# Kernel optimization log

Hardware: AMD Instinct MI355X
Metric: run time of the kernel (lower is better)

## Reference

```python
import jax, jax.numpy as jnp
import numpy as np

B, CIN, COUT, K, IH, IW = 2, 32, 32, 9, 256, 256
OH, OW = 512, 512


def setup_inputs() -> dict:
    key = jax.random.key(0)
    k0, k1, k2, k3 = jax.random.split(key, 4)
    stdv = 1.0 / np.sqrt(CIN * K)
    x = jax.random.normal(k0, (B, CIN, IH, IW), jnp.float32)
    weight = jax.random.uniform(k1, (CIN, COUT, K), jnp.float32, -stdv, stdv)
    bias = jax.random.uniform(k2, (COUT,), jnp.float32, -stdv, stdv)
    # continuous (x, y) coords into the OUTPUT plane; keep strictly inside so x0+1/y0+1 are valid
    sm = jax.random.uniform(k3, (IH, IW, K, 2), jnp.float32)
    scale = jnp.array([(OW - 1) * 0.999, (OH - 1) * 0.999], jnp.float32)
    sample_map = sm * scale
    return {"x": x, "weight": weight, "bias": bias, "sample_map": sample_map, "oh": OH, "ow": OW}


def reference(x, weight, bias, sample_map, oh, ow):
    Bb, Cin, Ih, Iw = x.shape
    Cout = weight.shape[1]
    Kk = weight.shape[2]
    P = Ih * Iw
    xf = x.reshape(Bb, Cin, P)
    # per-kernel-tap weight transform of every input pixel: [B, Cout, K, P]
    contrib = jnp.einsum('bip,iok->bokp', xf, weight)

    sx = sample_map[..., 0].reshape(P, Kk).T  # [K, P] x-coords in output
    sy = sample_map[..., 1].reshape(P, Kk).T  # [K, P] y-coords in output
    x0f = jnp.floor(sx)
    y0f = jnp.floor(sy)
    dx = sx - x0f
    dy = sy - y0f
    x0 = jnp.clip(x0f.astype(jnp.int32), 0, ow - 1)
    y0 = jnp.clip(y0f.astype(jnp.int32), 0, oh - 1)
    x1 = jnp.clip(x0 + 1, 0, ow - 1)
    y1 = jnp.clip(y0 + 1, 0, oh - 1)

    # bilinear splat weights and flat output indices for the 4 corners: [4, K, P]
    w = jnp.stack([(1 - dx) * (1 - dy), dx * (1 - dy), (1 - dx) * dy, dx * dy], 0)
    idx = jnp.stack([y0 * ow + x0, y0 * ow + x1, y1 * ow + x0, y1 * ow + x1], 0)

    vals = contrib[:, :, None, :, :] * w[None, None, :, :, :]  # [B, Cout, 4, K, P]
    out = jnp.zeros((Bb, Cout, oh * ow), vals.dtype).at[:, :, idx].add(vals)
    return out.reshape(Bb, Cout, oh, ow) + bias[None, :, None, None]
```

## Files before the change

kernel.cpp:

```cpp
#include <hip/hip_runtime.h>
#include <hip/hip_fp16.h>

#define CIN 32
#define COUT 32
#define KK 9
#define PIX 65536
#define OH 512
#define OW 512
#define OHOW (OH*OW)
#define NCH 64
#define TW 16
#define TH 4
#define TPX (TW*TH)
#define NTX (OW/TW)
#define NTY (OH/TH)
#define NTILE (NTX*NTY)
#define NBIN NTILE
#define NPK (PIX*KK)
#define CAP 384

#define OFF_CNT 0
#define OFF_WT  (256*1024)
#define OFF_ENT (512*1024)
#define OFF_CB  (OFF_ENT + (size_t)NBIN*CAP*8)
#define WS_NEED (OFF_CB + (size_t)NPK*NCH*2)

typedef __bf16    bf16x8 __attribute__((ext_vector_type(8)));
typedef _Float16  f16x8  __attribute__((ext_vector_type(8)));
typedef float     f32x4  __attribute__((ext_vector_type(4)));

__device__ __forceinline__ unsigned short f2h(float v)
{
    return __half_as_ushort(__float2half_rn(v));
}

__device__ __forceinline__ void corners(float sx, float sy,
    int& x0, int& y0, int& x1, int& y1, float& dx, float& dy)
{
    const float x0f = floorf(sx), y0f = floorf(sy);
    dx = sx - x0f; dy = sy - y0f;
    x0 = min(max((int)x0f, 0), OW - 1);
    y0 = min(max((int)y0f, 0), OH - 1);
    x1 = min(x0 + 1, OW - 1);
    y1 = min(y0 + 1, OH - 1);
}

__global__ __launch_bounds__(256) void k_wtb(
    const float* __restrict__ w, __bf16* __restrict__ wth, __bf16* __restrict__ wtl)
{
    const int t = blockIdx.x * 256 + threadIdx.x;
    if (t < KK * COUT * CIN) {
        const int i = t & 31;
        const int o = (t >> 5) & 31;
        const int k = t >> 10;
        const float v = w[(i * COUT + o) * KK + k];
        const __bf16 h = (__bf16)v;
        wth[t] = h;
        wtl[t] = (__bf16)(v - (float)h);
    }
}

__global__ __launch_bounds__(256, 1) void k_contrib4(
    const float* __restrict__ x, const __bf16* __restrict__ wth,
    const __bf16* __restrict__ wtl, const float* __restrict__ smap,
    unsigned short* __restrict__ cb, unsigned* __restrict__ cnt,
    uint2* __restrict__ ent)
{
    __shared__ __align__(16) unsigned short patch[4][2][16][72];
    const int tid = threadIdx.x, lane = tid & 63;
    const int wu = __builtin_amdgcn_readfirstlane(tid >> 6);
    const int p0 = blockIdx.x * 64;
    const int colp = lane & 15;
    const int q    = lane >> 4;
    const int cig  = q * 8;

    unsigned aS[3][4], aA[3][4], aR[3][4], aW[3];
    #pragma unroll
    for (int it = 0; it < 3; ++it) {
        const int idx = tid + it * 256;
        const bool vit = idx < 576;
        const int t = min(p0 * KK + idx, NPK - 1);
        const float sx = smap[2 * t], sy = smap[2 * t + 1];
        int x0, y0, x1, y1; float dx, dy;
        corners(sx, sy, x0, y0, x1, y1, dx, dy);
        const int g0 = x0 >> 4, g1 = x1 >> 4;
        const int t0 = y0 >> 2, t1 = y1 >> 2;
        aW[it] = (unsigned)f2h(dx) | ((unsigned)f2h(dy) << 16);
        const bool dg = (g1 != g0), dt = (t1 != t0);
        const bool cond[4] = { vit, vit && dg, vit && dt, vit && dg && dt };
        const int  tys[4]  = { t0, t0, t1, t1 };
        const int  gss[4]  = { g0, g1, g0, g1 };
        #pragma unroll
        for (int e = 0; e < 4; ++e) {
            unsigned slot = 0xFFFFFFFFu;
            const int bin = tys[e] * 32 + gss[e];
            const unsigned lxb = (unsigned)(x0 - gss[e] * TW + 1);
            const unsigned lyb = (unsigned)(y0 - tys[e] * TH + 1);
            if (cond[e]) slot = atomicAdd(&cnt[bin * 16], 1u);
            aS[it][e] = slot;
            aA[it][e] = (unsigned)bin * CAP;
            aR[it][e] = (unsigned)t | (lxb << 20) | (lyb << 25);
        }
    }

    bf16x8 xh[2], xl[2];
    #pragma unroll
    for (int b = 0; b < 2; ++b) {
        const int p = p0 + wu * 16 + colp;
        #pragma unroll
        for (int j = 0; j < 8; ++j) {
            const float v = x[(size_t)(b * 32 + cig + j) * PIX + p];
            const __bf16 h = (__bf16)v;
            xh[b][j] = h;
            xl[b][j] = (__bf16)(v - (float)h);
        }
    }

    const int pxr = lane >> 2, cc = lane & 3;
    for (int k = 0; k < KK; ++k) {
        const int kb = k & 1;
        const __bf16* wb = wth + k * (COUT * CIN);
        const __bf16* lb = wtl + k * (COUT * CIN);
        bf16x8 wh[2], wl[2];
        #pragma unroll
        for (int oh = 0; oh < 2; ++oh) {
            wh[oh] = *(const bf16x8*)(wb + (oh * 16 + colp) * 32 + cig);
            wl[oh] = *(const bf16x8*)(lb + (oh * 16 + colp) * 32 + cig);
        }
        #pragma unroll
        for (int cg = 0; cg < 4; ++cg) {
            const int b = cg >> 1, oh = cg & 1;
            f32x4 a = {0.f, 0.f, 0.f, 0.f};
            a = __builtin_amdgcn_mfma_f32_16x16x32_bf16(wh[oh], xh[b], a, 0, 0, 0);
            a = __builtin_amdgcn_mfma_f32_16x16x32_bf16(wl[oh], xh[b], a, 0, 0, 0);
            a = __builtin_amdgcn_mfma_f32_16x16x32_bf16(wh[oh], xl[b], a, 0, 0, 0);
            const unsigned d0 = (unsigned)f2h(a[0]) | ((unsigned)f2h(a[1]) << 16);
            const unsigned d1 = (unsigned)f2h(a[2]) | ((unsigned)f2h(a[3]) << 16);
            *(uint2*)&patch[wu][kb][colp][cg * 16 + q * 4] = make_uint2(d0, d1);
        }
        const uint4 a0 = *(const uint4*)&patch[wu][kb][pxr][cc * 8];
        const uint4 a1 = *(const uint4*)&patch[wu][kb][pxr][32 + cc * 8];
        unsigned short* dst = cb + (size_t)(p0 + wu * 16 + pxr) * 576 + k * 64 + cc * 8;
        *(uint4*)dst        = a0;
        *(uint4*)(dst + 32) = a1;
    }

    #pragma unroll
    for (int it = 0; it < 3; ++it) {
        #pragma unroll
        for (int e = 0; e < 4; ++e) {
            if (aS[it][e] < CAP)
                ent[(size_t)aA[it][e] + aS[it][e]] = make_uint2(aR[it][e], aW[it]);
        }
    }
}

__global__ __launch_bounds__(256, 4) void k_gather(
    const unsigned short* __restrict__ cb, const uint2* __restrict__ ent,
    const unsigned* __restrict__ cnt, const float* __restrict__ bias,
    float* __restrict__ out)
{
    __shared__ __align__(16) unsigned char smem[32768];
    const int tid = threadIdx.x, lane = tid & 63;
    const int wv = __builtin_amdgcn_readfirstlane(tid >> 6);
    const int bt = blockIdx.x;
    const int tx0 = (bt & 31) * TW;
    const int ty0 = (bt >> 5) * TH;

    const unsigned count = min(cnt[bt * 16], (unsigned)CAP);
    const uint2* eb = ent + (size_t)bt * CAP;
    const int nb = (int)(count + 63) >> 6;

    f32x4 acc[4] = {{0.f,0.f,0.f,0.f},{0.f,0.f,0.f,0.f},
                    {0.f,0.f,0.f,0.f},{0.f,0.f,0.f,0.f}};

    for (int it = 0; it <= nb; ++it) {
        const int bb = it & 1;
        unsigned short* Wb = (unsigned short*)(smem + bb * 8192);
        unsigned short* Cv = (unsigned short*)(smem + 16384 + bb * 8192);
        if (it < nb) {
            uint4* wq = (uint4*)Wb;
            const uint4 z = make_uint4(0u, 0u, 0u, 0u);
            wq[tid] = z; wq[tid + 256] = z;
        }
        __syncthreads();

        unsigned short u[16];
        if (it < nb) {
            {
                const int eL = tid >> 2, cn = tid & 3;
                const unsigned idx = (unsigned)(it * 64 + eL);
                if (idx < count) {
                    const uint2 r = eb[idx];
                    const int lx = (int)((r.x >> 20) & 31) - 1 + (cn & 1);
                    const int ly = (int)((r.x >> 25) & 7) - 1 + (cn >> 1);
                    if (((unsigned)lx < TW) & ((unsigned)ly < TH)) {
                        const float dx = __half2float(__ushort_as_half((unsigned short)(r.y & 0xFFFF)));
                        const float dy = __half2float(__ushort_as_half((unsigned short)(r.y >> 16)));
                        const float wx = (cn & 1) ? dx : 1.f - dx;
                        const float wy = (cn >> 1) ? dy : 1.f - dy;
                        const int px = ly * TW + lx;
                        Wb[px * 64 + (eL ^ ((px & 7) << 3))] = f2h(wx * wy);
                    }
                }
            }
            #pragma unroll
            for (int j = 0; j < 16; ++j) {
                const unsigned idx = (unsigned)(it * 64 + wv * 16 + j);
                unsigned short v = 0;
                if (idx < count) {
                    const unsigned row = eb[idx].x & 0xFFFFFu;
                    v = cb[((size_t)row << 6) + lane];
                }
                u[j] = v;
            }
        }
        if (it > 0) {
            const int pb = bb ^ 1;
            const unsigned short* Wp = (const unsigned short*)(smem + pb * 8192);
            const unsigned short* Cp = (const unsigned short*)(smem + 16384 + pb * 8192);
            const int m = lane & 15, kh = lane >> 4;
            const int px = wv * 16 + m;
            f16x8 af[2];
            #pragma unroll
            for (int kc = 0; kc < 2; ++kc)
                af[kc] = *(const f16x8*)(Wp + px * 64 + (((kc * 4 + kh) ^ (px & 7)) << 3));
            #pragma unroll
            for (int n = 0; n < 4; ++n) {
                const int ch = n * 16 + m;
                #pragma unroll
                for (int kc = 0; kc < 2; ++kc) {
                    const f16x8 bf = *(const f16x8*)(Cp + ch * 64 + (((kc * 4 + kh) ^ (ch & 7)) << 3));
                    acc[n] = __builtin_amdgcn_mfma_f32_16x16x32_f16(af[kc], bf, acc[n], 0, 0, 0);
                }
            }
        }
        if (it < nb) {
            uint4* cvq = (uint4*)Cv;
            const uint4 pk0 = make_uint4(
                (unsigned)u[0]  | ((unsigned)u[1]  << 16),
                (unsigned)u[2]  | ((unsigned)u[3]  << 16),
                (unsigned)u[4]  | ((unsigned)u[5]  << 16),
                (unsigned)u[6]  | ((unsigned)u[7]  << 16));
            const uint4 pk1 = make_uint4(
                (unsigned)u[8]  | ((unsigned)u[9]  << 16),
                (unsigned)u[10] | ((unsigned)u[11] << 16),
                (unsigned)u[12] | ((unsigned)u[13] << 16),
                (unsigned)u[14] | ((unsigned)u[15] << 16));
            cvq[lane * 8 + ((wv * 2)     ^ (lane & 7))] = pk0;
            cvq[lane * 8 + ((wv * 2 + 1) ^ (lane & 7))] = pk1;
        }
        __syncthreads();
    }

    float* stage = (float*)smem;
    #pragma unroll
    for (int n = 0; n < 4; ++n) {
        #pragma unroll
        for (int r = 0; r < 4; ++r)
            stage[(wv * 16 + (lane >> 4) * 4 + r) * 65 + n * 16 + (lane & 15)] = acc[n][r];
    }
    __syncthreads();
    const int py = lane >> 4, pxx = lane & 15;
    const size_t q = (size_t)(ty0 + py) * OW + tx0 + pxx;
    #pragma unroll
    for (int j = 0; j < 16; ++j) {
        const int c = wv * 16 + j;
        out[(size_t)c * OHOW + q] = stage[(py * 16 + pxx) * 65 + c] + bias[c & 31];
    }
}

__global__ __launch_bounds__(576) void mtc_scatter_direct(
    const float* __restrict__ x, const float* __restrict__ weight,
    const float* __restrict__ smap, float* __restrict__ acc)
{
    __shared__ float xs[64][68];
    __shared__ float sm[64 * KK * 2];
    const int t = threadIdx.x;
    const int p0 = blockIdx.x * 64;
    if (t < 512) {
        const int pp = t & 63, c0 = t >> 6;
        #pragma unroll
        for (int ch = 0; ch < 8; ++ch) {
            const int c = c0 + ch * 8;
            xs[pp][c] = x[(size_t)c * PIX + p0 + pp];
        }
    }
    for (int i = t; i < 64 * KK * 2; i += 576)
        sm[i] = smap[(size_t)p0 * (KK * 2) + i];
    const int k = t >> 6, lane = t & 63, b = lane >> 5, o = lane & 31;
    float wreg[CIN];
    #pragma unroll
    for (int i = 0; i < CIN; ++i) wreg[i] = weight[(i * COUT + o) * KK + k];
    __syncthreads();
    for (int pp = 0; pp < 64; ++pp) {
        const float sx = sm[(pp * KK + k) * 2], sy = sm[(pp * KK + k) * 2 + 1];
        int x0, y0, x1, y1; float dx, dy;
        corners(sx, sy, x0, y0, x1, y1, dx, dy);
        const float* xrow = &xs[pp][b * 32];
        float cv = 0.f;
        #pragma unroll
        for (int j = 0; j < 8; ++j) {
            const float4 xv = *(const float4*)(xrow + 4 * j);
            cv += xv.x * wreg[4*j] + xv.y * wreg[4*j+1] + xv.z * wreg[4*j+2] + xv.w * wreg[4*j+3];
        }
        const size_t base = (size_t)lane * OHOW;
        atomicAdd(&acc[base + y0 * OW + x0], cv * (1.f - dx) * (1.f - dy));
        atomicAdd(&acc[base + y0 * OW + x1], cv * dx * (1.f - dy));
        atomicAdd(&acc[base + y1 * OW + x0], cv * (1.f - dx) * dy);
        atomicAdd(&acc[base + y1 * OW + x1], cv * dx * dy);
    }
}

__global__ __launch_bounds__(256) void mtc_bias_add(
    float* __restrict__ out, const float* __restrict__ bias)
{
    const size_t i = (size_t)blockIdx.x * 256 + threadIdx.x;
    out[i] += bias[(i >> 18) & 31];
}

extern "C" void kernel_launch(void* const* d_in, const int* in_sizes, int n_in,
                              void* d_out, int out_size, void* d_ws, size_t ws_size,
                              hipStream_t stream) {
    const float* x      = (const float*)d_in[0];
    const float* weight = (const float*)d_in[1];
    const float* bias   = (const float*)d_in[2];
    const float* smap   = (const float*)d_in[3];
    float* out = (float*)d_out;
    char* ws = (char*)d_ws;

    if (ws_size >= WS_NEED) {
        unsigned* cnt = (unsigned*)(ws + OFF_CNT);
        __bf16* wth   = (__bf16*)(ws + OFF_WT);
        __bf16* wtl   = wth + KK * COUT * CIN;
        uint2* ent    = (uint2*)(ws + OFF_ENT);
        unsigned short* cb = (unsigned short*)(ws + OFF_CB);

        hipMemsetAsync(cnt, 0, NBIN * 16 * sizeof(unsigned), stream);
        k_wtb<<<(KK * COUT * CIN + 255) / 256, 256, 0, stream>>>(weight, wth, wtl);
        k_contrib4<<<PIX / 64, 256, 0, stream>>>(x, wth, wtl, smap, cb, cnt, ent);
        k_gather<<<NTILE, 256, 0, stream>>>(cb, ent, cnt, bias, out);
    } else {
        hipMemsetAsync(out, 0, (size_t)OHOW * NCH * sizeof(float), stream);
        mtc_scatter_direct<<<PIX / 64, 576, 0, stream>>>(x, weight, smap, out);
        mtc_bias_add<<<(OHOW * NCH) / 256, 256, 0, stream>>>(out, bias);
    }
}
```

Measured before the change: 183.3 us.

## Split bin counters into per-segment bins and stage entry lists in LDS

Each output-tile bin's atomic counter and entry list is split into 4 segments, chosen by contrib block index modulo 4, to spread atomic contention. The gather kernel merges the four segment lists into a shared-memory entry list once, then reads entries from LDS instead of global memory on every iteration. The contrib kernel also loads x earlier and double-buffers the per-tap weight loads in registers across a fully unrolled tap loop. In exchange, counters are packed densely instead of padded to 16 words, so neighbouring counters share cache lines. Each segment is capped at 96 entries, which risks silently dropping entries if the sample map is skewed.

```diff
diff --git a/kernel.cpp b/kernel.cpp
--- a/kernel.cpp
+++ b/kernel.cpp
@@ -17,12 +17,14 @@
 #define NTILE (NTX*NTY)
 #define NBIN NTILE
 #define NPK (PIX*KK)
-#define CAP 384
+#define NSEG 4
+#define SCAP 96
+#define CAPT (NSEG*SCAP)
 
 #define OFF_CNT 0
 #define OFF_WT  (256*1024)
 #define OFF_ENT (512*1024)
-#define OFF_CB  (OFF_ENT + (size_t)NBIN*CAP*8)
+#define OFF_CB  (OFF_ENT + (size_t)NBIN*NSEG*SCAP*8)
 #define WS_NEED (OFF_CB + (size_t)NPK*NCH*2)
 
 typedef __bf16    bf16x8 __attribute__((ext_vector_type(8)));
@@ -60,7 +62,7 @@
     }
 }
 
-__global__ __launch_bounds__(256, 1) void k_contrib4(
+__global__ __launch_bounds__(256, 1) void k_contrib5(
     const float* __restrict__ x, const __bf16* __restrict__ wth,
     const __bf16* __restrict__ wtl, const float* __restrict__ smap,
     unsigned short* __restrict__ cb, unsigned* __restrict__ cnt,
@@ -70,9 +72,29 @@
     const int tid = threadIdx.x, lane = tid & 63;
     const int wu = __builtin_amdgcn_readfirstlane(tid >> 6);
     const int p0 = blockIdx.x * 64;
+    const unsigned seg = blockIdx.x & 3;
     const int colp = lane & 15;
     const int q    = lane >> 4;
     const int cig  = q * 8;
+
+    bf16x8 xh[2], xl[2];
+    #pragma unroll
+    for (int b = 0; b < 2; ++b) {
+        const int p = p0 + wu * 16 + colp;
+        #pragma unroll
+        for (int j = 0; j < 8; ++j) {
+            const float v = x[(size_t)(b * 32 + cig + j) * PIX + p];
+            const __bf16 h = (__bf16)v;
+            xh[b][j] = h;
+            xl[b][j] = (__bf16)(v - (float)h);
+        }
+    }
+    bf16x8 wwh[2][2], wwl[2][2];
+    #pragma unroll
+    for (int oh = 0; oh < 2; ++oh) {
+        wwh[0][oh] = *(const bf16x8*)(wth + (oh * 16 + colp) * 32 + cig);
+        wwl[0][oh] = *(const bf16x8*)(wtl + (oh * 16 + colp) * 32 + cig);
+    }
 
     unsigned aS[3][4], aA[3][4], aR[3][4], aW[3];
     #pragma unroll
@@ -96,44 +118,34 @@
             const int bin = tys[e] * 32 + gss[e];
             const unsigned lxb = (unsigned)(x0 - gss[e] * TW + 1);
             const unsigned lyb = (unsigned)(y0 - tys[e] * TH + 1);
-            if (cond[e]) slot = atomicAdd(&cnt[bin * 16], 1u);
+            if (cond[e]) slot = atomicAdd(&cnt[seg * NBIN + bin], 1u);
             aS[it][e] = slot;
-            aA[it][e] = (unsigned)bin * CAP;
+            aA[it][e] = ((unsigned)bin * NSEG + seg) * SCAP;
             aR[it][e] = (unsigned)t | (lxb << 20) | (lyb << 25);
         }
     }
 
-    bf16x8 xh[2], xl[2];
-    #pragma unroll
-    for (int b = 0; b < 2; ++b) {
-        const int p = p0 + wu * 16 + colp;
-        #pragma unroll
-        for (int j = 0; j < 8; ++j) {
-            const float v = x[(size_t)(b * 32 + cig + j) * PIX + p];
-            const __bf16 h = (__bf16)v;
-            xh[b][j] = h;
-            xl[b][j] = (__bf16)(v - (float)h);
-        }
-    }
-
     const int pxr = lane >> 2, cc = lane & 3;
+    #pragma unroll
     for (int k = 0; k < KK; ++k) {
         const int kb = k & 1;
-        const __bf16* wb = wth + k * (COUT * CIN);
-        const __bf16* lb = wtl + k * (COUT * CIN);
-        bf16x8 wh[2], wl[2];
-        #pragma unroll
-        for (int oh = 0; oh < 2; ++oh) {
-            wh[oh] = *(const bf16x8*)(wb + (oh * 16 + colp) * 32 + cig);
-            wl[oh] = *(const bf16x8*)(lb + (oh * 16 + colp) * 32 + cig);
+        const int cur = k & 1, nxt = cur ^ 1;
+        if (k + 1 < KK) {
+            const __bf16* wb = wth + (k + 1) * (COUT * CIN);
+            const __bf16* lb = wtl + (k + 1) * (COUT * CIN);
+            #pragma unroll
+            for (int oh = 0; oh < 2; ++oh) {
+                wwh[nxt][oh] = *(const bf16x8*)(wb + (oh * 16 + colp) * 32 + cig);
+                wwl[nxt][oh] = *(const bf16x8*)(lb + (oh * 16 + colp) * 32 + cig);
+            }
         }
         #pragma unroll
         for (int cg = 0; cg < 4; ++cg) {
             const int b = cg >> 1, oh = cg & 1;
             f32x4 a = {0.f, 0.f, 0.f, 0.f};
-            a = __builtin_amdgcn_mfma_f32_16x16x32_bf16(wh[oh], xh[b], a, 0, 0, 0);
-            a = __builtin_amdgcn_mfma_f32_16x16x32_bf16(wl[oh], xh[b], a, 0, 0, 0);
-            a = __builtin_amdgcn_mfma_f32_16x16x32_bf16(wh[oh], xl[b], a, 0, 0, 0);
+            a = __builtin_amdgcn_mfma_f32_16x16x32_bf16(wwh[cur][oh], xh[b], a, 0, 0, 0);
+            a = __builtin_amdgcn_mfma_f32_16x16x32_bf16(wwl[cur][oh], xh[b], a, 0, 0, 0);
+            a = __builtin_amdgcn_mfma_f32_16x16x32_bf16(wwh[cur][oh], xl[b], a, 0, 0, 0);
             const unsigned d0 = (unsigned)f2h(a[0]) | ((unsigned)f2h(a[1]) << 16);
             const unsigned d1 = (unsigned)f2h(a[2]) | ((unsigned)f2h(a[3]) << 16);
             *(uint2*)&patch[wu][kb][colp][cg * 16 + q * 4] = make_uint2(d0, d1);
@@ -149,7 +161,7 @@
     for (int it = 0; it < 3; ++it) {
         #pragma unroll
         for (int e = 0; e < 4; ++e) {
-            if (aS[it][e] < CAP)
+            if (aS[it][e] < SCAP)
                 ent[(size_t)aA[it][e] + aS[it][e]] = make_uint2(aR[it][e], aW[it]);
         }
     }
@@ -161,14 +173,31 @@
     float* __restrict__ out)
 {
     __shared__ __align__(16) unsigned char smem[32768];
+    __shared__ __align__(16) uint2 elist[CAPT];
     const int tid = threadIdx.x, lane = tid & 63;
     const int wv = __builtin_amdgcn_readfirstlane(tid >> 6);
     const int bt = blockIdx.x;
     const int tx0 = (bt & 31) * TW;
     const int ty0 = (bt >> 5) * TH;
 
-    const unsigned count = min(cnt[bt * 16], (unsigned)CAP);
-    const uint2* eb = ent + (size_t)bt * CAP;
+    const unsigned c0 = min(cnt[0 * NBIN + bt], (unsigned)SCAP);
+    const unsigned c1 = min(cnt[1 * NBIN + bt], (unsigned)SCAP);
+    const unsigned c2 = min(cnt[2 * NBIN + bt], (unsigned)SCAP);
+    const unsigned c3 = min(cnt[3 * NBIN + bt], (unsigned)SCAP);
+    const unsigned o1 = c0, o2 = c0 + c1, o3 = o2 + c2;
+    const unsigned count = o3 + c3;
+    {
+        const uint2* e0 = ent + ((size_t)bt * NSEG + 0) * SCAP;
+        const uint2* e1 = ent + ((size_t)bt * NSEG + 1) * SCAP;
+        const uint2* e2 = ent + ((size_t)bt * NSEG + 2) * SCAP;
+        const uint2* e3 = ent + ((size_t)bt * NSEG + 3) * SCAP;
+        if ((unsigned)tid < c0) elist[tid]      = e0[tid];
+        if ((unsigned)tid < c1) elist[o1 + tid] = e1[tid];
+        if ((unsigned)tid < c2) elist[o2 + tid] = e2[tid];
+        if ((unsigned)tid < c3) elist[o3 + tid] = e3[tid];
+    }
+    __syncthreads();
+
     const int nb = (int)(count + 63) >> 6;
 
     f32x4 acc[4] = {{0.f,0.f,0.f,0.f},{0.f,0.f,0.f,0.f},
@@ -191,7 +220,7 @@
                 const int eL = tid >> 2, cn = tid & 3;
                 const unsigned idx = (unsigned)(it * 64 + eL);
                 if (idx < count) {
-                    const uint2 r = eb[idx];
+                    const uint2 r = elist[idx];
                     const int lx = (int)((r.x >> 20) & 31) - 1 + (cn & 1);
                     const int ly = (int)((r.x >> 25) & 7) - 1 + (cn >> 1);
                     if (((unsigned)lx < TW) & ((unsigned)ly < TH)) {
@@ -209,7 +238,7 @@
                 const unsigned idx = (unsigned)(it * 64 + wv * 16 + j);
                 unsigned short v = 0;
                 if (idx < count) {
-                    const unsigned row = eb[idx].x & 0xFFFFFu;
+                    const unsigned row = elist[idx].x & 0xFFFFFu;
                     v = cb[((size_t)row << 6) + lane];
                 }
                 u[j] = v;
@@ -336,9 +365,9 @@
         uint2* ent    = (uint2*)(ws + OFF_ENT);
         unsigned short* cb = (unsigned short*)(ws + OFF_CB);
 
-        hipMemsetAsync(cnt, 0, NBIN * 16 * sizeof(unsigned), stream);
+        hipMemsetAsync(cnt, 0, NSEG * NBIN * sizeof(unsigned), stream);
         k_wtb<<<(KK * COUT * CIN + 255) / 256, 256, 0, stream>>>(weight, wth, wtl);
-        k_contrib4<<<PIX / 64, 256, 0, stream>>>(x, wth, wtl, smap, cb, cnt, ent);
+        k_contrib5<<<PIX / 64, 256, 0, stream>>>(x, wth, wtl, smap, cb, cnt, ent);
         k_gather<<<NTILE, 256, 0, stream>>>(cb, ent, cnt, bias, out);
     } else {
         hipMemsetAsync(out, 0, (size_t)OHOW * NCH * sizeof(float), stream);
```

After: 169.5 us. 1.08x faster.
